# Kernel optimization log

Hardware: AMD Instinct MI355X
Metric: run time of the kernel (lower is better)

Reference implementation:

```python
import jax, jax.numpy as jnp
import numpy as np

MODEL_DIM = 1024
HEADS = 16
HEAD_DIM = MODEL_DIM // HEADS
SEQ = 1024


def setup_inputs() -> dict:
    key0 = jax.random.key(0)
    ks = jax.random.split(key0, 10)
    D, H, d, S = MODEL_DIM, HEADS, HEAD_DIM, SEQ
    s = 1.0 / np.sqrt(D)
    return {
        "value": jax.random.normal(ks[0], (S, D), dtype=jnp.float32),
        "key": jax.random.normal(ks[1], (S, D), dtype=jnp.float32),
        "query": jax.random.normal(ks[2], (S, D), dtype=jnp.float32),
        # per-head projection weights, torch Linear layout (out=d, in=D), stacked over heads
        "Wq": jax.random.uniform(ks[3], (H, d, D), jnp.float32, -s, s),
        "Wk": jax.random.uniform(ks[4], (H, d, D), jnp.float32, -s, s),
        "Wv": jax.random.uniform(ks[5], (H, d, D), jnp.float32, -s, s),
        # u, v biases: torch.rand -> uniform [0,1)
        "u": jax.random.uniform(ks[6], (H, d), dtype=jnp.float32),
        "v": jax.random.uniform(ks[7], (H, d), dtype=jnp.float32),
        "Wo": jax.random.uniform(ks[8], (D, D), jnp.float32, -s, s),
        "bo": jax.random.uniform(ks[9], (D,), jnp.float32, -s, s),
    }


def _rel_pos_R(d, Sq, Sk):
    # pos[i, j] = i - j (Transformer-XL style relative offsets)
    pos = (jnp.arange(Sq)[:, None] - jnp.arange(Sk)[None, :]).astype(jnp.float32)
    inv_freq = 10000.0 ** (-2.0 * jnp.arange(d // 2, dtype=jnp.float32) / d)  # (d/2,)
    ang = pos[None, :, :] * inv_freq[:, None, None]  # (d/2, Sq, Sk)
    # interleave: R[2i] = sin(ang_i), R[2i+1] = cos(ang_i)
    R = jnp.stack([jnp.sin(ang), jnp.cos(ang)], axis=1).reshape(d, Sq, Sk)
    return R


def reference(value, key, query, Wq, Wk, Wv, u, v, Wo, bo):
    # defaults of original forward: scale=True, mask=False
    H, d, D = Wq.shape
    Sq, Sk = query.shape[0], key.shape[0]
    q = jnp.einsum("hdD,sD->hsd", Wq, query)   # (H, Sq, d)
    k = jnp.einsum("hdD,tD->htd", Wk, key)     # (H, Sk, d)
    vals = jnp.einsum("hdD,tD->htd", Wv, value)  # (H, Sk, d)

    R = _rel_pos_R(d, Sq, Sk)  # (d, Sq, Sk)

    cc = jnp.einsum("hsd,htd->hst", q, k)       # content-content
    cp = jnp.einsum("hsd,dst->hst", q, R)       # content-position
    uk = jnp.einsum("hd,htd->ht", u, k)[:, None, :]  # global content bias
    vr = jnp.einsum("hd,dst->hst", v, R)        # global position bias

    att = (cc + cp + uk + vr) * (d ** -0.5)
    att = jax.nn.softmax(att, axis=2)

    out = jnp.einsum("hst,htd->hsd", att, vals)  # (H, Sq, d)
    out = out.transpose(1, 0, 2).reshape(Sq, H * d)  # concat heads along feature dim
    return out @ Wo.T + bo
```

## Files before the change

### kernel.cpp

```cpp
#include <hip/hip_runtime.h>
#include <math.h>

#define SQ 1024
#define DIM 1024
#define NH 16
#define HDIM 64

typedef short bf16x8 __attribute__((ext_vector_type(8)));
typedef float f32x4 __attribute__((ext_vector_type(4)));

__device__ __forceinline__ unsigned short f2bf(float x) {
  unsigned int u = __builtin_bit_cast(unsigned int, x);
  u += 0x7FFFu + ((u >> 16) & 1u);
  return (unsigned short)(u >> 16);
}
__device__ __forceinline__ unsigned int pkbf(float a, float b) {
  return (unsigned)f2bf(a) | ((unsigned)f2bf(b) << 16);
}

__global__ __launch_bounds__(256) void prep_kernel(
    const float* __restrict__ query, const float* __restrict__ key_,
    const float* __restrict__ value, const float* __restrict__ Wq,
    const float* __restrict__ Wk, const float* __restrict__ Wv,
    const float* __restrict__ Wo, unsigned short* __restrict__ bfin,
    unsigned short* __restrict__ Rc)
{
  const int b = blockIdx.x;
  if (b < 3584) {
    int gid = b * 256 + threadIdx.x;
    int seg = gid >> 17;
    int off = (gid & 131071) * 8;
    const float* s = seg == 0 ? query : seg == 1 ? key_ : seg == 2 ? value :
                     seg == 3 ? Wq : seg == 4 ? Wk : seg == 5 ? Wv : Wo;
    float4 a = *(const float4*)&s[off];
    float4 c = *(const float4*)&s[off + 4];
    uint4 o;
    o.x = pkbf(a.x, a.y); o.y = pkbf(a.z, a.w);
    o.z = pkbf(c.x, c.y); o.w = pkbf(c.z, c.w);
    *(uint4*)&bfin[(size_t)gid * 8] = o;
  } else {
    int gid = (b - 3584) * 256 + threadIdx.x;
    int p = gid >> 5, f = gid & 31;
    float pos = (float)(p - (SQ - 1));
    float invf = expf(-0.28782313662425575f * (float)f);
    float ang = pos * invf;
    Rc[p * HDIM + 2 * f]     = f2bf(sinf(ang));
    Rc[p * HDIM + 2 * f + 1] = f2bf(cosf(ang));
  }
}

__global__ __launch_bounds__(256) void gemm_qkv(
    const unsigned short* __restrict__ bfin,
    unsigned short* __restrict__ qu, unsigned short* __restrict__ qv,
    unsigned short* __restrict__ kkp, unsigned short* __restrict__ vvpT,
    const float* __restrict__ u, const float* __restrict__ v)
{
  __shared__ short As[64 * 72];
  __shared__ short Bs[64 * 72];
  const int z = blockIdx.z;
  const unsigned short* A = bfin + (size_t)z * (1 << 20);
  const unsigned short* B = bfin + (size_t)(3 + z) * (1 << 20);
  const int tid = threadIdx.x;
  const int bm = blockIdx.y * 64, bn = blockIdx.x * 64;
  const int w = tid >> 6, l = tid & 63, g = l >> 4, q = l & 15;
  const int wr = w >> 1, wc = w & 1;
  const int srow = tid >> 2, sc = (tid & 3) * 16;
  f32x4 acc[2][2] = {};

  for (int k0 = 0; k0 < DIM; k0 += 64) {
    __syncthreads();
    {
      const uint4* s0 = (const uint4*)&A[(bm + srow) * DIM + k0 + sc];
      *(uint4*)&As[srow * 72 + sc]     = s0[0];
      *(uint4*)&As[srow * 72 + sc + 8] = s0[1];
      const uint4* s1 = (const uint4*)&B[(bn + srow) * DIM + k0 + sc];
      *(uint4*)&Bs[srow * 72 + sc]     = s1[0];
      *(uint4*)&Bs[srow * 72 + sc + 8] = s1[1];
    }
    __syncthreads();
    #pragma unroll
    for (int ks = 0; ks < 2; ks++) {
      bf16x8 a0 = *(const bf16x8*)&As[(wr * 32 + q) * 72      + ks * 32 + g * 8];
      bf16x8 a1 = *(const bf16x8*)&As[(wr * 32 + 16 + q) * 72 + ks * 32 + g * 8];
      bf16x8 b0 = *(const bf16x8*)&Bs[(wc * 32 + q) * 72      + ks * 32 + g * 8];
      bf16x8 b1 = *(const bf16x8*)&Bs[(wc * 32 + 16 + q) * 72 + ks * 32 + g * 8];
      acc[0][0] = __builtin_amdgcn_mfma_f32_16x16x32_bf16(a0, b0, acc[0][0], 0, 0, 0);
      acc[0][1] = __builtin_amdgcn_mfma_f32_16x16x32_bf16(a0, b1, acc[0][1], 0, 0, 0);
      acc[1][0] = __builtin_amdgcn_mfma_f32_16x16x32_bf16(a1, b0, acc[1][0], 0, 0, 0);
      acc[1][1] = __builtin_amdgcn_mfma_f32_16x16x32_bf16(a1, b1, acc[1][1], 0, 0, 0);
    }
  }

  #pragma unroll
  for (int i = 0; i < 2; i++) {
    #pragma unroll
    for (int j = 0; j < 2; j++) {
      const int m0 = bm + wr * 32 + i * 16 + g * 4;
      const int n  = bn + wc * 32 + j * 16 + q;
      if (z == 0) {
        float uu = u[n], vv = v[n];
        #pragma unroll
        for (int r = 0; r < 4; r++) {
          qu[(m0 + r) * DIM + n] = f2bf((acc[i][j][r] + uu) * 0.125f);
          qv[(m0 + r) * DIM + n] = f2bf((acc[i][j][r] + vv) * 0.125f);
        }
      } else if (z == 1) {
        #pragma unroll
        for (int r = 0; r < 4; r++)
          kkp[(m0 + r) * DIM + n] = f2bf(acc[i][j][r]);
      } else {
        ushort4 pk;
        pk.x = f2bf(acc[i][j][0]); pk.y = f2bf(acc[i][j][1]);
        pk.z = f2bf(acc[i][j][2]); pk.w = f2bf(acc[i][j][3]);
        *(ushort4*)&vvpT[n * SQ + m0] = pk;
      }
    }
  }
}

__global__ __launch_bounds__(256) void gemm_out(
    const unsigned short* __restrict__ A, const unsigned short* __restrict__ B,
    float* __restrict__ out, const float* __restrict__ bo)
{
  __shared__ short As[64 * 72];
  __shared__ short Bs[64 * 72];
  const int tid = threadIdx.x;
  const int bm = blockIdx.y * 64, bn = blockIdx.x * 64;
  const int w = tid >> 6, l = tid & 63, g = l >> 4, q = l & 15;
  const int wr = w >> 1, wc = w & 1;
  const int srow = tid >> 2, sc = (tid & 3) * 16;
  f32x4 acc[2][2] = {};

  for (int k0 = 0; k0 < DIM; k0 += 64) {
    __syncthreads();
    {
      const uint4* s0 = (const uint4*)&A[(bm + srow) * DIM + k0 + sc];
      *(uint4*)&As[srow * 72 + sc]     = s0[0];
      *(uint4*)&As[srow * 72 + sc + 8] = s0[1];
      const uint4* s1 = (const uint4*)&B[(bn + srow) * DIM + k0 + sc];
      *(uint4*)&Bs[srow * 72 + sc]     = s1[0];
      *(uint4*)&Bs[srow * 72 + sc + 8] = s1[1];
    }
    __syncthreads();
    #pragma unroll
    for (int ks = 0; ks < 2; ks++) {
      bf16x8 a0 = *(const bf16x8*)&As[(wr * 32 + q) * 72      + ks * 32 + g * 8];
      bf16x8 a1 = *(const bf16x8*)&As[(wr * 32 + 16 + q) * 72 + ks * 32 + g * 8];
      bf16x8 b0 = *(const bf16x8*)&Bs[(wc * 32 + q) * 72      + ks * 32 + g * 8];
      bf16x8 b1 = *(const bf16x8*)&Bs[(wc * 32 + 16 + q) * 72 + ks * 32 + g * 8];
      acc[0][0] = __builtin_amdgcn_mfma_f32_16x16x32_bf16(a0, b0, acc[0][0], 0, 0, 0);
      acc[0][1] = __builtin_amdgcn_mfma_f32_16x16x32_bf16(a0, b1, acc[0][1], 0, 0, 0);
      acc[1][0] = __builtin_amdgcn_mfma_f32_16x16x32_bf16(a1, b0, acc[1][0], 0, 0, 0);
      acc[1][1] = __builtin_amdgcn_mfma_f32_16x16x32_bf16(a1, b1, acc[1][1], 0, 0, 0);
    }
  }

  #pragma unroll
  for (int i = 0; i < 2; i++) {
    #pragma unroll
    for (int j = 0; j < 2; j++) {
      const int m0 = bm + wr * 32 + i * 16 + g * 4;
      const int n  = bn + wc * 32 + j * 16 + q;
      float bb = bo[n];
      #pragma unroll
      for (int r = 0; r < 4; r++)
        out[(m0 + r) * DIM + n] = acc[i][j][r] + bb;
    }
  }
}

__global__ __launch_bounds__(256, 2) void attn_mfma(
    const unsigned short* __restrict__ qu, const unsigned short* __restrict__ qv,
    const unsigned short* __restrict__ kkp, const unsigned short* __restrict__ vvpT,
    const unsigned short* __restrict__ Rc, float* __restrict__ PO,
    float* __restrict__ ML)
{
  __shared__ short Ks[64 * 72];
  __shared__ short Vs[64 * 72];
  __shared__ short Rcs[128 * 72];
  __shared__ short Ps[64 * 72];
  __shared__ float Gs[64 * 84];

  const int tid = threadIdx.x;
  const int h  = blockIdx.x >> 4;
  const int s0 = (blockIdx.x & 15) * 64;
  const int th = blockIdx.y;
  const int w = tid >> 6, l = tid & 63, g = l >> 4, q = l & 15;
  const int col0 = h * HDIM;

  const int sw = s0 + w * 16 + q;
  bf16x8 qub[2], qvb[2];
  qub[0] = *(const bf16x8*)&qu[sw * DIM + col0 + g * 8];
  qub[1] = *(const bf16x8*)&qu[sw * DIM + col0 + 32 + g * 8];
  qvb[0] = *(const bf16x8*)&qv[sw * DIM + col0 + g * 8];
  qvb[1] = *(const bf16x8*)&qv[sw * DIM + col0 + 32 + g * 8];

  f32x4 accO[4] = {};
  float m_run = -1e30f, l_run = 0.f;

  const int srow = tid >> 2, sc = (tid & 3) * 16;
  const int rrow = tid >> 1, rc = (tid & 1) * 32;

  for (int t0 = th * 512; t0 < th * 512 + 512; t0 += 64) {
    __syncthreads();
    {
      const uint4* ksrc = (const uint4*)&kkp[(t0 + srow) * DIM + col0 + sc];
      *(uint4*)&Ks[srow * 72 + sc]     = ksrc[0];
      *(uint4*)&Ks[srow * 72 + sc + 8] = ksrc[1];
      const uint4* vsrc = (const uint4*)&vvpT[(col0 + srow) * SQ + t0 + sc];
      *(uint4*)&Vs[srow * 72 + sc]     = vsrc[0];
      *(uint4*)&Vs[srow * 72 + sc + 8] = vsrc[1];
      const int P0 = s0 - t0 + 960;
      const uint4* rsrc = (const uint4*)&Rc[(P0 + rrow) * HDIM + rc];
      *(uint4*)&Rcs[rrow * 72 + rc]      = rsrc[0];
      *(uint4*)&Rcs[rrow * 72 + rc + 8]  = rsrc[1];
      *(uint4*)&Rcs[rrow * 72 + rc + 16] = rsrc[2];
      *(uint4*)&Rcs[rrow * 72 + rc + 24] = rsrc[3];
    }
    __syncthreads();

    f32x4 accS[4] = {};
    f32x4 accG[5] = {};
    #pragma unroll
    for (int ks = 0; ks < 2; ks++) {
      #pragma unroll
      for (int tf = 0; tf < 4; tf++) {
        bf16x8 a = *(const bf16x8*)&Ks[(tf * 16 + q) * 72 + ks * 32 + g * 8];
        accS[tf] = __builtin_amdgcn_mfma_f32_16x16x32_bf16(a, qub[ks], accS[tf], 0, 0, 0);
      }
      #pragma unroll
      for (int pf = 0; pf < 5; pf++) {
        bf16x8 a = *(const bf16x8*)&Rcs[(w * 16 + pf * 16 + q) * 72 + ks * 32 + g * 8];
        accG[pf] = __builtin_amdgcn_mfma_f32_16x16x32_bf16(a, qvb[ks], accG[pf], 0, 0, 0);
      }
    }
    #pragma unroll
    for (int pf = 0; pf < 5; pf++)
      *(f32x4*)&Gs[(w * 16 + q) * 84 + pf * 16 + g * 4] = accG[pf];

    float pvals[16];
    float mx = -1e30f;
    #pragma unroll
    for (int tf = 0; tf < 4; tf++) {
      #pragma unroll
      for (int r = 0; r < 4; r++) {
        int t_rel = tf * 16 + g * 4 + r;
        float sval = accS[tf][r] + Gs[(w * 16 + q) * 84 + (q - t_rel + 63)];
        pvals[tf * 4 + r] = sval;
        mx = fmaxf(mx, sval);
      }
    }
    mx = fmaxf(mx, __shfl_xor(mx, 16));
    mx = fmaxf(mx, __shfl_xor(mx, 32));
    float m_new = fmaxf(m_run, mx);
    float scale = __expf(m_run - m_new);
    float rsum = 0.f;
    #pragma unroll
    for (int i = 0; i < 16; i++) {
      float p = __expf(pvals[i] - m_new);
      pvals[i] = p;
      rsum += p;
    }
    rsum += __shfl_xor(rsum, 16);
    rsum += __shfl_xor(rsum, 32);
    l_run = l_run * scale + rsum;
    m_run = m_new;
    #pragma unroll
    for (int df = 0; df < 4; df++) {
      #pragma unroll
      for (int r = 0; r < 4; r++) accO[df][r] *= scale;
    }
    #pragma unroll
    for (int tf = 0; tf < 4; tf++) {
      unsigned int lo = pkbf(pvals[tf * 4 + 0], pvals[tf * 4 + 1]);
      unsigned int hi = pkbf(pvals[tf * 4 + 2], pvals[tf * 4 + 3]);
      *(uint2*)&Ps[(w * 16 + q) * 72 + tf * 16 + g * 4] = make_uint2(lo, hi);
    }
    #pragma unroll
    for (int ks = 0; ks < 2; ks++) {
      bf16x8 b = *(const bf16x8*)&Ps[(w * 16 + q) * 72 + ks * 32 + g * 8];
      #pragma unroll
      for (int df = 0; df < 4; df++) {
        bf16x8 a = *(const bf16x8*)&Vs[(df * 16 + q) * 72 + ks * 32 + g * 8];
        accO[df] = __builtin_amdgcn_mfma_f32_16x16x32_bf16(a, b, accO[df], 0, 0, 0);
      }
    }
  }

  const int tile = blockIdx.x * 2 + th;
  float* POt = PO + (size_t)tile * 4096;
  const int sl = w * 16 + q;
  #pragma unroll
  for (int df = 0; df < 4; df++)
    *(f32x4*)&POt[sl * 64 + df * 16 + g * 4] = accO[df];
  if (g == 0) {
    ML[tile * 128 + sl * 2]     = m_run;
    ML[tile * 128 + sl * 2 + 1] = l_run;
  }
}

__global__ __launch_bounds__(256) void attn_combine(
    const float* __restrict__ PO, const float* __restrict__ ML,
    unsigned short* __restrict__ attout)
{
  int gid = blockIdx.x * 256 + threadIdx.x;
  int s  = gid >> 8;
  int c  = (gid & 255) * 4;
  int h  = c >> 6;
  int sb = s >> 6, sl = s & 63;
  int tA = (h * 16 + sb) * 2, tB = tA + 1;
  float mA = ML[tA * 128 + sl * 2], lA = ML[tA * 128 + sl * 2 + 1];
  float mB = ML[tB * 128 + sl * 2], lB = ML[tB * 128 + sl * 2 + 1];
  float m = fmaxf(mA, mB);
  float wA = __expf(mA - m), wB = __expf(mB - m);
  float inv = 1.f / (lA * wA + lB * wB);
  wA *= inv; wB *= inv;
  int dl = c & 63;
  float4 a = *(const float4*)&PO[(size_t)tA * 4096 + sl * 64 + dl];
  float4 b = *(const float4*)&PO[(size_t)tB * 4096 + sl * 64 + dl];
  uint2 o;
  o.x = pkbf(a.x * wA + b.x * wB, a.y * wA + b.y * wB);
  o.y = pkbf(a.z * wA + b.z * wB, a.w * wA + b.w * wB);
  *(uint2*)&attout[s * DIM + c] = o;
}

extern "C" void kernel_launch(void* const* d_in, const int* in_sizes, int n_in,
                              void* d_out, int out_size, void* d_ws, size_t ws_size,
                              hipStream_t stream) {
  const float* value = (const float*)d_in[0];
  const float* key   = (const float*)d_in[1];
  const float* query = (const float*)d_in[2];
  const float* Wq    = (const float*)d_in[3];
  const float* Wk    = (const float*)d_in[4];
  const float* Wv    = (const float*)d_in[5];
  const float* u     = (const float*)d_in[6];
  const float* v     = (const float*)d_in[7];
  const float* Wo    = (const float*)d_in[8];
  const float* bo    = (const float*)d_in[9];
  float* out = (float*)d_out;

  unsigned short* ws = (unsigned short*)d_ws;
  unsigned short* bfin   = ws;
  unsigned short* qu_p   = bfin   + 7 * (1 << 20);
  unsigned short* qv_p   = qu_p   + (1 << 20);
  unsigned short* kkp    = qv_p   + (1 << 20);
  unsigned short* vvpT   = kkp    + (1 << 20);
  unsigned short* attout = vvpT   + (1 << 20);
  unsigned short* Rc     = attout + (1 << 20);
  float* PO = (float*)(Rc + 2048 * 64);
  float* ML = PO + (size_t)512 * 4096;

  prep_kernel<<<3840, 256, 0, stream>>>(query, key, value, Wq, Wk, Wv, Wo, bfin, Rc);

  dim3 gqkv(16, 16, 3);
  gemm_qkv<<<gqkv, 256, 0, stream>>>(bfin, qu_p, qv_p, kkp, vvpT, u, v);

  dim3 gattn(NH * (SQ / 64), 2);
  attn_mfma<<<gattn, 256, 0, stream>>>(qu_p, qv_p, kkp, vvpT, Rc, PO, ML);
  attn_combine<<<1024, 256, 0, stream>>>(PO, ML, attout);

  dim3 gg(16, 16);
  gemm_out<<<gg, 256, 0, stream>>>(attout, bfin + 6 * (1 << 20), out, bo);
}
```

Before: 158.0 us.

## Prefetch next K-tile into registers and double-buffer LDS in GEMMs and attention

Both GEMM kernels now use double-buffered shared tiles. The next K-slice is loaded into registers before the MFMA work on the current slice and written to the alternate buffer afterward, leaving one barrier per iteration. The attention kernel prefetches the next K/V/R tiles into registers during compute and stores them after a barrier. The aim is to hide global-load latency behind matrix math, at the cost of more registers, which may lower occupancy. The attention kernel's launch-bounds hint for a minimum of two blocks per CU is also dropped, so the compiler is no longer held to that register budget.

```diff
diff --git a/kernel.cpp b/kernel.cpp
--- a/kernel.cpp
+++ b/kernel.cpp
@@ -55,8 +55,8 @@
     unsigned short* __restrict__ kkp, unsigned short* __restrict__ vvpT,
     const float* __restrict__ u, const float* __restrict__ v)
 {
-  __shared__ short As[64 * 72];
-  __shared__ short Bs[64 * 72];
+  __shared__ short As[2][64 * 72];
+  __shared__ short Bs[2][64 * 72];
   const int z = blockIdx.z;
   const unsigned short* A = bfin + (size_t)z * (1 << 20);
   const unsigned short* B = bfin + (size_t)(3 + z) * (1 << 20);
@@ -65,29 +65,47 @@
   const int w = tid >> 6, l = tid & 63, g = l >> 4, q = l & 15;
   const int wr = w >> 1, wc = w & 1;
   const int srow = tid >> 2, sc = (tid & 3) * 16;
+  const unsigned short* Arow = A + (bm + srow) * DIM + sc;
+  const unsigned short* Brow = B + (bn + srow) * DIM + sc;
   f32x4 acc[2][2] = {};
 
+  uint4 a0 = *(const uint4*)&Arow[0];
+  uint4 a1 = *(const uint4*)&Arow[8];
+  uint4 b0 = *(const uint4*)&Brow[0];
+  uint4 b1 = *(const uint4*)&Brow[8];
+  *(uint4*)&As[0][srow * 72 + sc]     = a0;
+  *(uint4*)&As[0][srow * 72 + sc + 8] = a1;
+  *(uint4*)&Bs[0][srow * 72 + sc]     = b0;
+  *(uint4*)&Bs[0][srow * 72 + sc + 8] = b1;
+  __syncthreads();
+
+  #pragma unroll 2
   for (int k0 = 0; k0 < DIM; k0 += 64) {
-    __syncthreads();
-    {
-      const uint4* s0 = (const uint4*)&A[(bm + srow) * DIM + k0 + sc];
-      *(uint4*)&As[srow * 72 + sc]     = s0[0];
-      *(uint4*)&As[srow * 72 + sc + 8] = s0[1];
-      const uint4* s1 = (const uint4*)&B[(bn + srow) * DIM + k0 + sc];
-      *(uint4*)&Bs[srow * 72 + sc]     = s1[0];
-      *(uint4*)&Bs[srow * 72 + sc + 8] = s1[1];
-    }
-    __syncthreads();
+    const int cur = (k0 >> 6) & 1;
+    const bool more = (k0 + 64 < DIM);
+    if (more) {
+      a0 = *(const uint4*)&Arow[k0 + 64];
+      a1 = *(const uint4*)&Arow[k0 + 64 + 8];
+      b0 = *(const uint4*)&Brow[k0 + 64];
+      b1 = *(const uint4*)&Brow[k0 + 64 + 8];
+    }
     #pragma unroll
     for (int ks = 0; ks < 2; ks++) {
-      bf16x8 a0 = *(const bf16x8*)&As[(wr * 32 + q) * 72      + ks * 32 + g * 8];
-      bf16x8 a1 = *(const bf16x8*)&As[(wr * 32 + 16 + q) * 72 + ks * 32 + g * 8];
-      bf16x8 b0 = *(const bf16x8*)&Bs[(wc * 32 + q) * 72      + ks * 32 + g * 8];
-      bf16x8 b1 = *(const bf16x8*)&Bs[(wc * 32 + 16 + q) * 72 + ks * 32 + g * 8];
-      acc[0][0] = __builtin_amdgcn_mfma_f32_16x16x32_bf16(a0, b0, acc[0][0], 0, 0, 0);
-      acc[0][1] = __builtin_amdgcn_mfma_f32_16x16x32_bf16(a0, b1, acc[0][1], 0, 0, 0);
-      acc[1][0] = __builtin_amdgcn_mfma_f32_16x16x32_bf16(a1, b0, acc[1][0], 0, 0, 0);
-      acc[1][1] = __builtin_amdgcn_mfma_f32_16x16x32_bf16(a1, b1, acc[1][1], 0, 0, 0);
+      bf16x8 fa0 = *(const bf16x8*)&As[cur][(wr * 32 + q) * 72      + ks * 32 + g * 8];
+      bf16x8 fa1 = *(const bf16x8*)&As[cur][(wr * 32 + 16 + q) * 72 + ks * 32 + g * 8];
+      bf16x8 fb0 = *(const bf16x8*)&Bs[cur][(wc * 32 + q) * 72      + ks * 32 + g * 8];
+      bf16x8 fb1 = *(const bf16x8*)&Bs[cur][(wc * 32 + 16 + q) * 72 + ks * 32 + g * 8];
+      acc[0][0] = __builtin_amdgcn_mfma_f32_16x16x32_bf16(fa0, fb0, acc[0][0], 0, 0, 0);
+      acc[0][1] = __builtin_amdgcn_mfma_f32_16x16x32_bf16(fa0, fb1, acc[0][1], 0, 0, 0);
+      acc[1][0] = __builtin_amdgcn_mfma_f32_16x16x32_bf16(fa1, fb0, acc[1][0], 0, 0, 0);
+      acc[1][1] = __builtin_amdgcn_mfma_f32_16x16x32_bf16(fa1, fb1, acc[1][1], 0, 0, 0);
+    }
+    if (more) {
+      *(uint4*)&As[cur ^ 1][srow * 72 + sc]     = a0;
+      *(uint4*)&As[cur ^ 1][srow * 72 + sc + 8] = a1;
+      *(uint4*)&Bs[cur ^ 1][srow * 72 + sc]     = b0;
+      *(uint4*)&Bs[cur ^ 1][srow * 72 + sc + 8] = b1;
+      __syncthreads();
     }
   }
 
@@ -122,36 +140,54 @@
     const unsigned short* __restrict__ A, const unsigned short* __restrict__ B,
     float* __restrict__ out, const float* __restrict__ bo)
 {
-  __shared__ short As[64 * 72];
-  __shared__ short Bs[64 * 72];
+  __shared__ short As[2][64 * 72];
+  __shared__ short Bs[2][64 * 72];
   const int tid = threadIdx.x;
   const int bm = blockIdx.y * 64, bn = blockIdx.x * 64;
   const int w = tid >> 6, l = tid & 63, g = l >> 4, q = l & 15;
   const int wr = w >> 1, wc = w & 1;
   const int srow = tid >> 2, sc = (tid & 3) * 16;
+  const unsigned short* Arow = A + (bm + srow) * DIM + sc;
+  const unsigned short* Brow = B + (bn + srow) * DIM + sc;
   f32x4 acc[2][2] = {};
 
+  uint4 a0 = *(const uint4*)&Arow[0];
+  uint4 a1 = *(const uint4*)&Arow[8];
+  uint4 b0 = *(const uint4*)&Brow[0];
+  uint4 b1 = *(const uint4*)&Brow[8];
+  *(uint4*)&As[0][srow * 72 + sc]     = a0;
+  *(uint4*)&As[0][srow * 72 + sc + 8] = a1;
+  *(uint4*)&Bs[0][srow * 72 + sc]     = b0;
+  *(uint4*)&Bs[0][srow * 72 + sc + 8] = b1;
+  __syncthreads();
+
+  #pragma unroll 2
   for (int k0 = 0; k0 < DIM; k0 += 64) {
-    __syncthreads();
-    {
-      const uint4* s0 = (const uint4*)&A[(bm + srow) * DIM + k0 + sc];
-      *(uint4*)&As[srow * 72 + sc]     = s0[0];
-      *(uint4*)&As[srow * 72 + sc + 8] = s0[1];
-      const uint4* s1 = (const uint4*)&B[(bn + srow) * DIM + k0 + sc];
-      *(uint4*)&Bs[srow * 72 + sc]     = s1[0];
-      *(uint4*)&Bs[srow * 72 + sc + 8] = s1[1];
-    }
-    __syncthreads();
+    const int cur = (k0 >> 6) & 1;
+    const bool more = (k0 + 64 < DIM);
+    if (more) {
+      a0 = *(const uint4*)&Arow[k0 + 64];
+      a1 = *(const uint4*)&Arow[k0 + 64 + 8];
+      b0 = *(const uint4*)&Brow[k0 + 64];
+      b1 = *(const uint4*)&Brow[k0 + 64 + 8];
+    }
     #pragma unroll
     for (int ks = 0; ks < 2; ks++) {
-      bf16x8 a0 = *(const bf16x8*)&As[(wr * 32 + q) * 72      + ks * 32 + g * 8];
-      bf16x8 a1 = *(const bf16x8*)&As[(wr * 32 + 16 + q) * 72 + ks * 32 + g * 8];
-      bf16x8 b0 = *(const bf16x8*)&Bs[(wc * 32 + q) * 72      + ks * 32 + g * 8];
-      bf16x8 b1 = *(const bf16x8*)&Bs[(wc * 32 + 16 + q) * 72 + ks * 32 + g * 8];
-      acc[0][0] = __builtin_amdgcn_mfma_f32_16x16x32_bf16(a0, b0, acc[0][0], 0, 0, 0);
-      acc[0][1] = __builtin_amdgcn_mfma_f32_16x16x32_bf16(a0, b1, acc[0][1], 0, 0, 0);
-      acc[1][0] = __builtin_amdgcn_mfma_f32_16x16x32_bf16(a1, b0, acc[1][0], 0, 0, 0);
-      acc[1][1] = __builtin_amdgcn_mfma_f32_16x16x32_bf16(a1, b1, acc[1][1], 0, 0, 0);
+      bf16x8 fa0 = *(const bf16x8*)&As[cur][(wr * 32 + q) * 72      + ks * 32 + g * 8];
+      bf16x8 fa1 = *(const bf16x8*)&As[cur][(wr * 32 + 16 + q) * 72 + ks * 32 + g * 8];
+      bf16x8 fb0 = *(const bf16x8*)&Bs[cur][(wc * 32 + q) * 72      + ks * 32 + g * 8];
+      bf16x8 fb1 = *(const bf16x8*)&Bs[cur][(wc * 32 + 16 + q) * 72 + ks * 32 + g * 8];
+      acc[0][0] = __builtin_amdgcn_mfma_f32_16x16x32_bf16(fa0, fb0, acc[0][0], 0, 0, 0);
+      acc[0][1] = __builtin_amdgcn_mfma_f32_16x16x32_bf16(fa0, fb1, acc[0][1], 0, 0, 0);
+      acc[1][0] = __builtin_amdgcn_mfma_f32_16x16x32_bf16(fa1, fb0, acc[1][0], 0, 0, 0);
+      acc[1][1] = __builtin_amdgcn_mfma_f32_16x16x32_bf16(fa1, fb1, acc[1][1], 0, 0, 0);
+    }
+    if (more) {
+      *(uint4*)&As[cur ^ 1][srow * 72 + sc]     = a0;
+      *(uint4*)&As[cur ^ 1][srow * 72 + sc + 8] = a1;
+      *(uint4*)&Bs[cur ^ 1][srow * 72 + sc]     = b0;
+      *(uint4*)&Bs[cur ^ 1][srow * 72 + sc + 8] = b1;
+      __syncthreads();
     }
   }
 
@@ -169,7 +205,7 @@
   }
 }
 
-__global__ __launch_bounds__(256, 2) void attn_mfma(
+__global__ __launch_bounds__(256) void attn_mfma(
     const unsigned short* __restrict__ qu, const unsigned short* __restrict__ qv,
     const unsigned short* __restrict__ kkp, const unsigned short* __restrict__ vvpT,
     const unsigned short* __restrict__ Rc, float* __restrict__ PO,
@@ -201,23 +237,45 @@
   const int srow = tid >> 2, sc = (tid & 3) * 16;
   const int rrow = tid >> 1, rc = (tid & 1) * 32;
 
-  for (int t0 = th * 512; t0 < th * 512 + 512; t0 += 64) {
-    __syncthreads();
-    {
-      const uint4* ksrc = (const uint4*)&kkp[(t0 + srow) * DIM + col0 + sc];
-      *(uint4*)&Ks[srow * 72 + sc]     = ksrc[0];
-      *(uint4*)&Ks[srow * 72 + sc + 8] = ksrc[1];
-      const uint4* vsrc = (const uint4*)&vvpT[(col0 + srow) * SQ + t0 + sc];
-      *(uint4*)&Vs[srow * 72 + sc]     = vsrc[0];
-      *(uint4*)&Vs[srow * 72 + sc + 8] = vsrc[1];
-      const int P0 = s0 - t0 + 960;
-      const uint4* rsrc = (const uint4*)&Rc[(P0 + rrow) * HDIM + rc];
-      *(uint4*)&Rcs[rrow * 72 + rc]      = rsrc[0];
-      *(uint4*)&Rcs[rrow * 72 + rc + 8]  = rsrc[1];
-      *(uint4*)&Rcs[rrow * 72 + rc + 16] = rsrc[2];
-      *(uint4*)&Rcs[rrow * 72 + rc + 24] = rsrc[3];
-    }
-    __syncthreads();
+  const int tstart = th * 512, tend = th * 512 + 512;
+
+  uint4 kr0, kr1, vr0, vr1, rr0, rr1, rr2, rr3;
+  {
+    const int t0 = tstart;
+    kr0 = *(const uint4*)&kkp[(t0 + srow) * DIM + col0 + sc];
+    kr1 = *(const uint4*)&kkp[(t0 + srow) * DIM + col0 + sc + 8];
+    vr0 = *(const uint4*)&vvpT[(col0 + srow) * SQ + t0 + sc];
+    vr1 = *(const uint4*)&vvpT[(col0 + srow) * SQ + t0 + sc + 8];
+    const int P0 = s0 - t0 + 960;
+    rr0 = *(const uint4*)&Rc[(P0 + rrow) * HDIM + rc];
+    rr1 = *(const uint4*)&Rc[(P0 + rrow) * HDIM + rc + 8];
+    rr2 = *(const uint4*)&Rc[(P0 + rrow) * HDIM + rc + 16];
+    rr3 = *(const uint4*)&Rc[(P0 + rrow) * HDIM + rc + 24];
+    *(uint4*)&Ks[srow * 72 + sc]      = kr0;
+    *(uint4*)&Ks[srow * 72 + sc + 8]  = kr1;
+    *(uint4*)&Vs[srow * 72 + sc]      = vr0;
+    *(uint4*)&Vs[srow * 72 + sc + 8]  = vr1;
+    *(uint4*)&Rcs[rrow * 72 + rc]      = rr0;
+    *(uint4*)&Rcs[rrow * 72 + rc + 8]  = rr1;
+    *(uint4*)&Rcs[rrow * 72 + rc + 16] = rr2;
+    *(uint4*)&Rcs[rrow * 72 + rc + 24] = rr3;
+  }
+  __syncthreads();
+
+  for (int t0 = tstart; t0 < tend; t0 += 64) {
+    const bool more = (t0 + 64 < tend);
+    if (more) {
+      const int tn = t0 + 64;
+      kr0 = *(const uint4*)&kkp[(tn + srow) * DIM + col0 + sc];
+      kr1 = *(const uint4*)&kkp[(tn + srow) * DIM + col0 + sc + 8];
+      vr0 = *(const uint4*)&vvpT[(col0 + srow) * SQ + tn + sc];
+      vr1 = *(const uint4*)&vvpT[(col0 + srow) * SQ + tn + sc + 8];
+      const int P0 = s0 - tn + 960;
+      rr0 = *(const uint4*)&Rc[(P0 + rrow) * HDIM + rc];
+      rr1 = *(const uint4*)&Rc[(P0 + rrow) * HDIM + rc + 8];
+      rr2 = *(const uint4*)&Rc[(P0 + rrow) * HDIM + rc + 16];
+      rr3 = *(const uint4*)&Rc[(P0 + rrow) * HDIM + rc + 24];
+    }
 
     f32x4 accS[4] = {};
     f32x4 accG[5] = {};
@@ -284,6 +342,19 @@
         bf16x8 a = *(const bf16x8*)&Vs[(df * 16 + q) * 72 + ks * 32 + g * 8];
         accO[df] = __builtin_amdgcn_mfma_f32_16x16x32_bf16(a, b, accO[df], 0, 0, 0);
       }
+    }
+
+    if (more) {
+      __syncthreads();
+      *(uint4*)&Ks[srow * 72 + sc]      = kr0;
+      *(uint4*)&Ks[srow * 72 + sc + 8]  = kr1;
+      *(uint4*)&Vs[srow * 72 + sc]      = vr0;
+      *(uint4*)&Vs[srow * 72 + sc + 8]  = vr1;
+      *(uint4*)&Rcs[rrow * 72 + rc]      = rr0;
+      *(uint4*)&Rcs[rrow * 72 + rc + 8]  = rr1;
+      *(uint4*)&Rcs[rrow * 72 + rc + 16] = rr2;
+      *(uint4*)&Rcs[rrow * 72 + rc + 24] = rr3;
+      __syncthreads();
     }
   }
 
```

New measurement: 142.0 us. 1.11x faster.
